# Performance work log

Measured on AMD Instinct MI355X. Metric: run time of the kernel, lower is better.

Reference implementation:

```python
import jax, jax.numpy as jnp
import numpy as np

N, T, D = 64, 2048, 256


def setup_inputs() -> dict:
    key = jax.random.key(0)
    k1, k2, k3, k4 = jax.random.split(key, 4)
    query = jax.random.normal(k1, (N, D), dtype=jnp.float32)
    key_t = jax.random.normal(k2, (N, T, D), dtype=jnp.float32)
    value = jax.random.normal(k3, (N, T, D), dtype=jnp.float32)
    lens = jax.random.randint(k4, (N,), 1, T + 1, dtype=jnp.int64)  # valid lengths in [1, T]
    return {"query": query, "key": key_t, "value": value, "lens": lens}


def reference(query, key, value, lens):
    # energy[n, t] = <key[n, t, :], query[n, :]>
    energy = jnp.einsum("ntd,nd->nt", key, query)
    attention = jax.nn.softmax(energy, axis=1)  # [N, T]
    # mask out positions >= lens[n], then renormalize over valid positions
    attention_mask = (jnp.arange(T)[None, :] < lens[:, None]).astype(attention.dtype)
    mask_attention = attention * attention_mask
    norm_attention = mask_attention / jnp.sum(mask_attention, axis=1, keepdims=True)
    # context[n, d] = sum_t norm_attention[n, t] * value[n, t, d]
    context = jnp.einsum("nt,ntd->nd", norm_attention, value)
    return (context, norm_attention)
```

## Files before the change

### kernel.cpp

```cpp
#include <hip/hip_runtime.h>


#define N_B 64
#define T_S 2048
#define D_S 256
#define TPB 256
#define RC 64

__global__ __launch_bounds__(TPB) void energy_kernel(
    const float* __restrict__ q, const float* __restrict__ k,
    const int* __restrict__ lens, float* __restrict__ e) {
  const int n = blockIdx.y;
  const int L = lens[n];
  const int t0 = blockIdx.x * RC;
  if (t0 >= L) return;
  const int tend = min(t0 + RC, L);
  const int lane = threadIdx.x & 63;
  const int wave = threadIdx.x >> 6;

  const float4 qv = reinterpret_cast<const float4*>(q + (size_t)n * D_S)[lane];
  const float* kbase = k + (size_t)n * T_S * D_S;
  float* erow = e + (size_t)n * T_S;

  int t = t0 + wave;
  for (; t + 4 < tend; t += 8) {
    const float4 a =
        reinterpret_cast<const float4*>(kbase + (size_t)t * D_S)[lane];
    const float4 b =
        reinterpret_cast<const float4*>(kbase + (size_t)(t + 4) * D_S)[lane];
    float s0 = a.x * qv.x + a.y * qv.y + a.z * qv.z + a.w * qv.w;
    float s1 = b.x * qv.x + b.y * qv.y + b.z * qv.z + b.w * qv.w;
#pragma unroll
    for (int off = 32; off > 0; off >>= 1) {
      s0 += __shfl_xor(s0, off, 64);
      s1 += __shfl_xor(s1, off, 64);
    }
    if (lane == 0) {
      erow[t] = s0;
      erow[t + 4] = s1;
    }
  }
  if (t < tend) {
    const float4 a =
        reinterpret_cast<const float4*>(kbase + (size_t)t * D_S)[lane];
    float s0 = a.x * qv.x + a.y * qv.y + a.z * qv.z + a.w * qv.w;
#pragma unroll
    for (int off = 32; off > 0; off >>= 1) s0 += __shfl_xor(s0, off, 64);
    if (lane == 0) erow[t] = s0;
  }
}

__global__ __launch_bounds__(TPB) void stats_kernel(
    const int* __restrict__ lens, const float* __restrict__ e,
    float2* __restrict__ mz) {
  const int n = blockIdx.x;
  const int L = lens[n];
  const float* erow = e + (size_t)n * T_S;
  const int tid = threadIdx.x;
  __shared__ float red[4];

  float m = -1e30f;
  for (int t = tid; t < L; t += TPB) m = fmaxf(m, erow[t]);
#pragma unroll
  for (int off = 32; off > 0; off >>= 1) m = fmaxf(m, __shfl_xor(m, off, 64));
  if ((tid & 63) == 0) red[tid >> 6] = m;
  __syncthreads();
  m = fmaxf(fmaxf(red[0], red[1]), fmaxf(red[2], red[3]));
  __syncthreads();

  float z = 0.f;
  for (int t = tid; t < L; t += TPB) z += __expf(erow[t] - m);
#pragma unroll
  for (int off = 32; off > 0; off >>= 1) z += __shfl_xor(z, off, 64);
  if ((tid & 63) == 0) red[tid >> 6] = z;
  __syncthreads();
  if (tid == 0) {
    const float Z = red[0] + red[1] + red[2] + red[3];
    mz[n] = make_float2(m, 1.0f / Z);
  }
}

__global__ __launch_bounds__(TPB) void ctx_kernel(
    const float* __restrict__ v, const int* __restrict__ lens,
    const float* __restrict__ e, const float2* __restrict__ mz,
    float* __restrict__ out_ctx, float* __restrict__ out_attn) {
  const int n = blockIdx.y;
  const int L = lens[n];
  const int t0 = blockIdx.x * RC;
  const int tid = threadIdx.x;

  __shared__ float a_sh[RC];
  __shared__ float4 part[TPB];

  const float2 s = mz[n];
  if (tid < RC) {
    const int t = t0 + tid;
    const float a = (t < L) ? __expf(e[(size_t)n * T_S + t] - s.x) * s.y : 0.f;
    out_attn[(size_t)n * T_S + t] = a;
    a_sh[tid] = a;
  }
  __syncthreads();
  if (t0 >= L) return;

  const int nv = min(RC, L - t0);
  const int dg = tid & 63;
  const int tg = tid >> 6;
  const float* vbase = v + (size_t)n * T_S * D_S + (size_t)t0 * D_S;

  float4 acc0 = {0.f, 0.f, 0.f, 0.f}, acc1 = {0.f, 0.f, 0.f, 0.f};
  int j = tg;
  for (; j + 4 < nv; j += 8) {
    const float4 v0 =
        reinterpret_cast<const float4*>(vbase + (size_t)j * D_S)[dg];
    const float4 v1 =
        reinterpret_cast<const float4*>(vbase + (size_t)(j + 4) * D_S)[dg];
    const float a0 = a_sh[j], a1 = a_sh[j + 4];
    acc0.x = fmaf(a0, v0.x, acc0.x);
    acc0.y = fmaf(a0, v0.y, acc0.y);
    acc0.z = fmaf(a0, v0.z, acc0.z);
    acc0.w = fmaf(a0, v0.w, acc0.w);
    acc1.x = fmaf(a1, v1.x, acc1.x);
    acc1.y = fmaf(a1, v1.y, acc1.y);
    acc1.z = fmaf(a1, v1.z, acc1.z);
    acc1.w = fmaf(a1, v1.w, acc1.w);
  }
  if (j < nv) {
    const float4 v0 =
        reinterpret_cast<const float4*>(vbase + (size_t)j * D_S)[dg];
    const float a0 = a_sh[j];
    acc0.x = fmaf(a0, v0.x, acc0.x);
    acc0.y = fmaf(a0, v0.y, acc0.y);
    acc0.z = fmaf(a0, v0.z, acc0.z);
    acc0.w = fmaf(a0, v0.w, acc0.w);
  }
  acc0.x += acc1.x;
  acc0.y += acc1.y;
  acc0.z += acc1.z;
  acc0.w += acc1.w;

  part[tid] = acc0;
  __syncthreads();
  if (tg == 0) {
    float4 r = part[dg];
    const float4 r1 = part[dg + 64], r2 = part[dg + 128], r3 = part[dg + 192];
    r.x += r1.x + r2.x + r3.x;
    r.y += r1.y + r2.y + r3.y;
    r.z += r1.z + r2.z + r3.z;
    r.w += r1.w + r2.w + r3.w;
    float* dst = out_ctx + (size_t)n * D_S + dg * 4;
    atomicAdd(dst + 0, r.x);
    atomicAdd(dst + 1, r.y);
    atomicAdd(dst + 2, r.z);
    atomicAdd(dst + 3, r.w);
  }
}

extern "C" void kernel_launch(void* const* d_in, const int* in_sizes, int n_in,
                              void* d_out, int out_size, void* d_ws,
                              size_t ws_size, hipStream_t stream) {
  const float* query = (const float*)d_in[0];
  const float* key = (const float*)d_in[1];
  const float* value = (const float*)d_in[2];
  const int* lens = (const int*)d_in[3];

  float* out_ctx = (float*)d_out;
  float* out_attn = (float*)d_out + N_B * D_S;
  float* e = (float*)d_ws;
  float2* mz = (float2*)((float*)d_ws + (size_t)N_B * T_S);

  const dim3 grid(T_S / RC, N_B);

  hipMemsetAsync(out_ctx, 0, (size_t)N_B * D_S * sizeof(float), stream);

  energy_kernel<<<grid, TPB, 0, stream>>>(query, key, lens, e);
  stats_kernel<<<N_B, TPB, 0, stream>>>(lens, e, mz);
  ctx_kernel<<<grid, TPB, 0, stream>>>(value, lens, e, mz, out_ctx, out_attn);
}
```

Baseline: 266.9 us.

## Fuse energy, softmax and context into one split-softmax kernel plus merge

Replaces the three-kernel pipeline (energy, global stats, context) with a single per-chunk kernel. Each chunk computes its energies in shared memory, a local max and sum of exponentials, unnormalized probabilities, and a partial context vector. A small merge kernel then rescales the chunks with flash-decoding style log-sum-exp combination to produce the final attention and context. This removes the energy round trip through global memory, one kernel launch, the memset and the atomics, at the cost of a partial-context workspace and an extra rescale pass over the attention row.

```diff
diff --git a/kernel.cpp b/kernel.cpp
--- a/kernel.cpp
+++ b/kernel.cpp
@@ -6,22 +6,32 @@
 #define D_S 256
 #define TPB 256
 #define RC 64
+#define NC (T_S / RC)
 
-__global__ __launch_bounds__(TPB) void energy_kernel(
+__global__ __launch_bounds__(TPB) void fused_kernel(
     const float* __restrict__ q, const float* __restrict__ k,
-    const int* __restrict__ lens, float* __restrict__ e) {
+    const float* __restrict__ v, const int* __restrict__ lens,
+    float* __restrict__ p_out, float2* __restrict__ mzc,
+    float* __restrict__ Oc) {
   const int n = blockIdx.y;
+  const int c = blockIdx.x;
   const int L = lens[n];
-  const int t0 = blockIdx.x * RC;
+  const int t0 = c * RC;
   if (t0 >= L) return;
   const int tend = min(t0 + RC, L);
-  const int lane = threadIdx.x & 63;
-  const int wave = threadIdx.x >> 6;
+  const int tid = threadIdx.x;
+  const int lane = tid & 63;
+  const int wave = tid >> 6;
+
+  __shared__ float e_sh[RC];
+  __shared__ float p_sh[RC];
+  __shared__ float4 part[TPB];
+
+  if (tid < RC) e_sh[tid] = -1e30f;
+  __syncthreads();
 
   const float4 qv = reinterpret_cast<const float4*>(q + (size_t)n * D_S)[lane];
   const float* kbase = k + (size_t)n * T_S * D_S;
-  float* erow = e + (size_t)n * T_S;
-
   int t = t0 + wave;
   for (; t + 4 < tend; t += 8) {
     const float4 a =
@@ -36,8 +46,8 @@
       s1 += __shfl_xor(s1, off, 64);
     }
     if (lane == 0) {
-      erow[t] = s0;
-      erow[t + 4] = s1;
+      e_sh[t - t0] = s0;
+      e_sh[t + 4 - t0] = s1;
     }
   }
   if (t < tend) {
@@ -46,65 +56,28 @@
     float s0 = a.x * qv.x + a.y * qv.y + a.z * qv.z + a.w * qv.w;
 #pragma unroll
     for (int off = 32; off > 0; off >>= 1) s0 += __shfl_xor(s0, off, 64);
-    if (lane == 0) erow[t] = s0;
+    if (lane == 0) e_sh[t - t0] = s0;
   }
-}
-
-__global__ __launch_bounds__(TPB) void stats_kernel(
-    const int* __restrict__ lens, const float* __restrict__ e,
-    float2* __restrict__ mz) {
-  const int n = blockIdx.x;
-  const int L = lens[n];
-  const float* erow = e + (size_t)n * T_S;
-  const int tid = threadIdx.x;
-  __shared__ float red[4];
-
-  float m = -1e30f;
-  for (int t = tid; t < L; t += TPB) m = fmaxf(m, erow[t]);
-#pragma unroll
-  for (int off = 32; off > 0; off >>= 1) m = fmaxf(m, __shfl_xor(m, off, 64));
-  if ((tid & 63) == 0) red[tid >> 6] = m;
-  __syncthreads();
-  m = fmaxf(fmaxf(red[0], red[1]), fmaxf(red[2], red[3]));
   __syncthreads();
 
-  float z = 0.f;
-  for (int t = tid; t < L; t += TPB) z += __expf(erow[t] - m);
+  if (wave == 0) {
+    const float e = e_sh[lane];
+    float m = e;
 #pragma unroll
-  for (int off = 32; off > 0; off >>= 1) z += __shfl_xor(z, off, 64);
-  if ((tid & 63) == 0) red[tid >> 6] = z;
-  __syncthreads();
-  if (tid == 0) {
-    const float Z = red[0] + red[1] + red[2] + red[3];
-    mz[n] = make_float2(m, 1.0f / Z);
-  }
-}
-
-__global__ __launch_bounds__(TPB) void ctx_kernel(
-    const float* __restrict__ v, const int* __restrict__ lens,
-    const float* __restrict__ e, const float2* __restrict__ mz,
-    float* __restrict__ out_ctx, float* __restrict__ out_attn) {
-  const int n = blockIdx.y;
-  const int L = lens[n];
-  const int t0 = blockIdx.x * RC;
-  const int tid = threadIdx.x;
-
-  __shared__ float a_sh[RC];
-  __shared__ float4 part[TPB];
-
-  const float2 s = mz[n];
-  if (tid < RC) {
-    const int t = t0 + tid;
-    const float a = (t < L) ? __expf(e[(size_t)n * T_S + t] - s.x) * s.y : 0.f;
-    out_attn[(size_t)n * T_S + t] = a;
-    a_sh[tid] = a;
+    for (int off = 32; off > 0; off >>= 1) m = fmaxf(m, __shfl_xor(m, off, 64));
+    const float pv = __expf(e - m);
+    float z = pv;
+#pragma unroll
+    for (int off = 32; off > 0; off >>= 1) z += __shfl_xor(z, off, 64);
+    p_sh[lane] = pv;
+    p_out[(size_t)n * T_S + t0 + lane] = pv;
+    if (lane == 0) mzc[n * NC + c] = make_float2(m, z);
   }
   __syncthreads();
-  if (t0 >= L) return;
 
-  const int nv = min(RC, L - t0);
   const int dg = tid & 63;
   const int tg = tid >> 6;
+  const int nv = tend - t0;
   const float* vbase = v + (size_t)n * T_S * D_S + (size_t)t0 * D_S;
 
   float4 acc0 = {0.f, 0.f, 0.f, 0.f}, acc1 = {0.f, 0.f, 0.f, 0.f};
@@ -114,7 +87,7 @@
         reinterpret_cast<const float4*>(vbase + (size_t)j * D_S)[dg];
     const float4 v1 =
         reinterpret_cast<const float4*>(vbase + (size_t)(j + 4) * D_S)[dg];
-    const float a0 = a_sh[j], a1 = a_sh[j + 4];
+    const float a0 = p_sh[j], a1 = p_sh[j + 4];
     acc0.x = fmaf(a0, v0.x, acc0.x);
     acc0.y = fmaf(a0, v0.y, acc0.y);
     acc0.z = fmaf(a0, v0.z, acc0.z);
@@ -127,7 +100,7 @@
   if (j < nv) {
     const float4 v0 =
         reinterpret_cast<const float4*>(vbase + (size_t)j * D_S)[dg];
-    const float a0 = a_sh[j];
+    const float a0 = p_sh[j];
     acc0.x = fmaf(a0, v0.x, acc0.x);
     acc0.y = fmaf(a0, v0.y, acc0.y);
     acc0.z = fmaf(a0, v0.z, acc0.z);
@@ -147,12 +120,50 @@
     r.y += r1.y + r2.y + r3.y;
     r.z += r1.z + r2.z + r3.z;
     r.w += r1.w + r2.w + r3.w;
-    float* dst = out_ctx + (size_t)n * D_S + dg * 4;
-    atomicAdd(dst + 0, r.x);
-    atomicAdd(dst + 1, r.y);
-    atomicAdd(dst + 2, r.z);
-    atomicAdd(dst + 3, r.w);
+    reinterpret_cast<float4*>(Oc + ((size_t)(n * NC + c)) * D_S)[dg] = r;
   }
+}
+
+__global__ __launch_bounds__(TPB) void merge_kernel(
+    const int* __restrict__ lens, const float* __restrict__ p_in,
+    const float2* __restrict__ mzc, const float* __restrict__ Oc,
+    float* __restrict__ out_ctx, float* __restrict__ out_attn) {
+  const int n = blockIdx.x;
+  const int L = lens[n];
+  const int nc = (L + RC - 1) / RC;
+  const int tid = threadIdx.x;
+  __shared__ float s_sh[NC];
+
+  if (tid < 64) {
+    float m = -1e30f, z = 0.f;
+    if (tid < nc) {
+      const float2 mz = mzc[n * NC + tid];
+      m = mz.x;
+      z = mz.y;
+    }
+    float M = m;
+#pragma unroll
+    for (int off = 32; off > 0; off >>= 1) M = fmaxf(M, __shfl_xor(M, off, 64));
+    const float sc = __expf(m - M);
+    float zs = z * sc;
+#pragma unroll
+    for (int off = 32; off > 0; off >>= 1) zs += __shfl_xor(zs, off, 64);
+    if (tid < NC) s_sh[tid] = sc / zs;
+  }
+  __syncthreads();
+
+#pragma unroll
+  for (int i = 0; i < T_S / TPB; ++i) {
+    const int t = i * TPB + tid;
+    const float a = (t < L) ? p_in[(size_t)n * T_S + t] * s_sh[t >> 6] : 0.f;
+    out_attn[(size_t)n * T_S + t] = a;
+  }
+
+  float acc = 0.f;
+  const float* ob = Oc + (size_t)n * NC * D_S + tid;
+#pragma unroll
+  for (int c2 = 0; c2 < NC; ++c2) acc = fmaf(s_sh[c2], ob[c2 * D_S], acc);
+  out_ctx[(size_t)n * D_S + tid] = acc;
 }
 
 extern "C" void kernel_launch(void* const* d_in, const int* in_sizes, int n_in,
@@ -165,14 +176,12 @@
 
   float* out_ctx = (float*)d_out;
   float* out_attn = (float*)d_out + N_B * D_S;
-  float* e = (float*)d_ws;
-  float2* mz = (float2*)((float*)d_ws + (size_t)N_B * T_S);
 
-  const dim3 grid(T_S / RC, N_B);
+  float* p = (float*)d_ws;
+  float2* mzc = (float2*)(p + (size_t)N_B * T_S);
+  float* Oc = (float*)(mzc + N_B * NC);
 
-  hipMemsetAsync(out_ctx, 0, (size_t)N_B * D_S * sizeof(float), stream);
-
-  energy_kernel<<<grid, TPB, 0, stream>>>(query, key, lens, e);
-  stats_kernel<<<N_B, TPB, 0, stream>>>(lens, e, mz);
-  ctx_kernel<<<grid, TPB, 0, stream>>>(value, lens, e, mz, out_ctx, out_attn);
+  const dim3 grid(NC, N_B);
+  fused_kernel<<<grid, TPB, 0, stream>>>(query, key, value, lens, p, mzc, Oc);
+  merge_kernel<<<N_B, TPB, 0, stream>>>(lens, p, mzc, Oc, out_ctx, out_attn);
 }
```

New measurement: 260.2 us. 1.03x faster.
